# Kernel optimization log

Measured on AMD Instinct MI355X. Metric: run time of the kernel, lower is better.

## Reference

```python
import jax, jax.numpy as jnp
import numpy as np

N_HOPS = 2
TOPK = 10
LAMBDA = 0.5  # lambda_coeff
N_ENT = 8192
N_USR = 16384
CHANNEL = 64
N_EDGE = 1000000
NNZ = 500000
N_REL = 9


def _l2norm(x, eps=1e-12):
    # F.normalize: x / max(||x||, eps) per row
    n = jnp.linalg.norm(x, axis=-1, keepdims=True)
    return x / jnp.maximum(n, eps)


def build_adj(context, topk):
    n = context.shape[0]
    cn = context / jnp.linalg.norm(context, axis=-1, keepdims=True)
    sim = cn @ cn.T                                   # [N,N]
    knn_val, knn_ind = jax.lax.top_k(sim, topk)        # [N,topk]
    rows = jnp.repeat(jnp.arange(n), topk)
    cols = knn_ind.reshape(-1)
    vals = knn_val.reshape(-1)
    rowsum = knn_val.sum(axis=1)                       # sparse row sums
    dinv = rowsum ** -0.5
    vals = dinv[rows] * vals * dinv[cols]              # D^-1/2 A D^-1/2
    return jnp.zeros((n, n), context.dtype).at[rows, cols].add(vals)


def aggregate(entity_emb, user_emb, head, tail, i_rows, i_cols, inter_vals, weight, edge_type):
    n_ent = entity_emb.shape[0]
    n_usr = user_emb.shape[0]
    rel = weight[edge_type - 1]                        # [E,C]
    h_emb = entity_emb[head]
    t_emb = entity_emb[tail]
    neigh = t_emb * rel                                # [E,C]
    # attention weight: (||h*r|| * ||t*r||)^2 per edge
    att = (jnp.linalg.norm(h_emb * rel, axis=1) * jnp.linalg.norm(t_emb * rel, axis=1)) ** 2
    # scatter_softmax over head segments
    m = jax.ops.segment_max(att, head, num_segments=n_ent)
    e = jnp.exp(att - m[head])
    denom = jax.ops.segment_sum(e, head, num_segments=n_ent)
    w = (e / denom[head])[:, None]                     # [E,1], broadcast == expand
    entity_agg = jax.ops.segment_sum(w * neigh, head, num_segments=n_ent)
    # sparse mm: interact_mat @ entity_emb
    user_agg = jax.ops.segment_sum(inter_vals[:, None] * entity_emb[i_cols], i_rows, num_segments=n_usr)
    score = jax.nn.softmax(user_emb @ weight.T, axis=-1)
    user_agg = user_agg + (score @ weight) * user_agg
    return entity_agg, user_agg


def setup_inputs() -> dict:
    key = jax.random.key(0)
    k = jax.random.split(key, 7)
    user_emb = jax.random.normal(k[0], (N_USR, CHANNEL), jnp.float32) * 0.1
    entity_emb = jax.random.normal(k[1], (N_ENT, CHANNEL), jnp.float32) * 0.1
    edge_index = jax.random.randint(k[2], (2, N_EDGE), 0, N_ENT)
    edge_type = jax.random.randint(k[3], (N_EDGE,), 0, N_REL - 1) + 1  # in [1, n_relations-1]
    inter_rows = jax.random.randint(k[4], (NNZ,), 0, N_USR)
    inter_cols = jax.random.randint(k[5], (NNZ,), 0, N_ENT)
    inter_indices = jnp.stack([inter_rows, inter_cols], axis=0)
    inter_vals = jax.random.uniform(k[6], (NNZ,), jnp.float32)
    # xavier-uniform-like relation weight
    bound = float(np.sqrt(6.0 / (N_REL - 1 + CHANNEL)))
    weight = jax.random.uniform(jax.random.fold_in(key, 7), (N_REL - 1, CHANNEL), jnp.float32, -bound, bound)
    return {"user_emb": user_emb, "entity_emb": entity_emb, "edge_index": edge_index,
            "edge_type": edge_type, "inter_indices": inter_indices,
            "inter_vals": inter_vals, "weight": weight}


def reference(user_emb, entity_emb, edge_index, edge_type, inter_indices, inter_vals, weight):
    head, tail = edge_index[0], edge_index[1]
    i_rows, i_cols = inter_indices[0], inter_indices[1]
    origin_item_adj = build_adj(entity_emb, TOPK)
    entity_res_emb = entity_emb
    user_res_emb = user_emb
    for _ in range(N_HOPS):
        entity_emb, user_emb = aggregate(entity_emb, user_emb, head, tail,
                                         i_rows, i_cols, inter_vals, weight, edge_type)
        entity_emb = _l2norm(entity_emb)
        user_emb = _l2norm(user_emb)
        entity_res_emb = entity_res_emb + entity_emb
        user_res_emb = user_res_emb + user_emb
    item_adj = (1.0 - LAMBDA) * build_adj(entity_res_emb, TOPK) + LAMBDA * origin_item_adj
    return entity_res_emb, user_res_emb, item_adj
```

## Files before the change

kernel.cpp:

```cpp
#include <hip/hip_runtime.h>
#include <hip/hip_bf16.h>

#define N_ENT   8192
#define N_USR   16384
#define CH      64
#define N_EDGEC 1000000
#define NNZC    500000
#define TOPKC   10
#define NRELM1  8
#define KSPLIT  384
#define BKS     96
#define LDSP    104
#define NTILE   64

typedef __bf16 bf16x8 __attribute__((ext_vector_type(8)));
typedef float  f32x4  __attribute__((ext_vector_type(4)));

static __device__ __forceinline__ float waveReduceSum(float v){
#pragma unroll
  for(int o=1;o<64;o<<=1) v += __shfl_xor(v,o,64);
  return v;
}
static __device__ __forceinline__ float waveReduceMax(float v){
#pragma unroll
  for(int o=1;o<64;o<<=1) v = fmaxf(v, __shfl_xor(v,o,64));
  return v;
}
static __device__ __forceinline__ unsigned long long u64max(unsigned long long a, unsigned long long b){
  return a>b? a: b;
}
static __device__ __forceinline__ unsigned mapf(float v){
  unsigned u = __float_as_uint(v);
  return (u & 0x80000000u) ? ~u : (u | 0x80000000u);
}
static __device__ __forceinline__ float unmapf(unsigned mk){
  unsigned uo = (mk & 0x80000000u) ? (mk ^ 0x80000000u) : ~mk;
  return __uint_as_float(uo);
}
static __device__ __forceinline__ ushort f2bf(float x){
  unsigned u = __float_as_uint(x);
  return (ushort)((u + 0x7FFFu + ((u>>16)&1u)) >> 16);
}
static __device__ __forceinline__ float bf2f(ushort h){
  return __uint_as_float((unsigned)h<<16);
}

__global__ void k_hist(const int* __restrict__ keys, int n, int* __restrict__ hist){
  int i = blockIdx.x*blockDim.x + threadIdx.x;
  int stride = gridDim.x*blockDim.x;
  for(; i<n; i+=stride) atomicAdd(&hist[keys[i]], 1);
}

__global__ __launch_bounds__(1024) void k_scan(const int* __restrict__ hist,
                                               int* __restrict__ start,
                                               int* __restrict__ cursor, int n){
  __shared__ int part[1024];
  int t = threadIdx.x;
  int chunk = n/1024;
  int base = t*chunk;
  int s = 0;
  for(int i=0;i<chunk;i++) s += hist[base+i];
  part[t] = s; __syncthreads();
  for(int off=1; off<1024; off<<=1){
    int v = (t>=off) ? part[t-off] : 0;
    __syncthreads();
    part[t] += v;
    __syncthreads();
  }
  int run = (t==0) ? 0 : part[t-1];
  for(int i=0;i<chunk;i++){
    start[base+i] = run; cursor[base+i] = run;
    run += hist[base+i];
  }
  if(t==1023) start[n] = run;
}

__global__ void k_scatter_sortE(const int* __restrict__ head,
                                const int* __restrict__ tail,
                                const int* __restrict__ etype, int n,
                                int* __restrict__ cursor, int* __restrict__ trS){
  int i = blockIdx.x*blockDim.x + threadIdx.x;
  int stride = gridDim.x*blockDim.x;
  for(; i<n; i+=stride){
    int pos = atomicAdd(&cursor[head[i]], 1);
    trS[pos] = (tail[i] & 8191) | ((etype[i]-1)<<13);
  }
}

__global__ void k_scatter_sortU(const int* __restrict__ irows,
                                const int* __restrict__ icols,
                                const float* __restrict__ ivals, int n,
                                int* __restrict__ cursor,
                                int* __restrict__ icolsS, float* __restrict__ ivalsS){
  int i = blockIdx.x*blockDim.x + threadIdx.x;
  int stride = gridDim.x*blockDim.x;
  for(; i<n; i+=stride){
    int pos = atomicAdd(&cursor[irows[i]], 1);
    icolsS[pos] = icols[i];
    ivalsS[pos] = ivals[i];
  }
}

__global__ __launch_bounds__(256) void k_split(const float* __restrict__ in,
                                               ushort* __restrict__ outA,
                                               ushort* __restrict__ outB){
  int wave = threadIdx.x>>6, lane = threadIdx.x&63;
  int r = blockIdx.x*4 + wave;
  float v = in[(size_t)r*CH+lane];
  float ss = waveReduceSum(v*v);
  float x = v / sqrtf(ss);
  ushort h = f2bf(x);
  float r1 = x - bf2f(h);
  ushort m = f2bf(r1);
  float r2 = r1 - bf2f(m);
  ushort l = f2bf(r2);
  ushort* oA = outA + (size_t)r*KSPLIT;
  ushort* oB = outB + (size_t)r*KSPLIT;
  oA[lane]     =h; oA[64+lane] =h; oA[128+lane]=m;
  oA[192+lane] =l; oA[256+lane]=h; oA[320+lane]=m;
  oB[lane]     =h; oB[64+lane] =m; oB[128+lane]=h;
  oB[192+lane] =h; oB[256+lane]=l; oB[320+lane]=m;
}

__global__ __launch_bounds__(256) void k_gemm_bf16(const ushort* __restrict__ A,
                                                   const ushort* __restrict__ B,
                                                   float* __restrict__ C,
                                                   float* __restrict__ rowmax){
  __shared__ ushort As[128*LDSP];
  __shared__ ushort Bs[128*LDSP];
  const int tid = threadIdx.x, lane = tid&63, wid = tid>>6;
  const int bi = blockIdx.y*128, bj = blockIdx.x*128;
  const int wr = (wid>>1)*64, wc = (wid&1)*64;
  const int r16 = lane&15, kg = lane>>4;

  f32x4 acc[4][4] = {};

  const uint4* gA = (const uint4*)A + (size_t)bi*(KSPLIT/8);
  const uint4* gB = (const uint4*)B + (size_t)bj*(KSPLIT/8);
  const int row2 = tid>>1, half = tid&1;

  for(int s=0; s<KSPLIT/BKS; ++s){
    __syncthreads();
#pragma unroll
    for(int jj=0;jj<6;jj++){
      *(uint4*)&As[row2*LDSP + half*48 + jj*8] = gA[row2*(KSPLIT/8) + s*12 + half*6 + jj];
      *(uint4*)&Bs[row2*LDSP + half*48 + jj*8] = gB[row2*(KSPLIT/8) + s*12 + half*6 + jj];
    }
    __syncthreads();
#pragma unroll
    for(int kk=0;kk<3;kk++){
      bf16x8 a[4], b[4];
#pragma unroll
      for(int m=0;m<4;m++)
        a[m] = *(const bf16x8*)&As[(wr+m*16+r16)*LDSP + kk*32 + kg*8];
#pragma unroll
      for(int n=0;n<4;n++)
        b[n] = *(const bf16x8*)&Bs[(wc+n*16+r16)*LDSP + kk*32 + kg*8];
#pragma unroll
      for(int m=0;m<4;m++)
#pragma unroll
        for(int n=0;n<4;n++)
          acc[m][n] = __builtin_amdgcn_mfma_f32_16x16x32_bf16(a[m], b[n], acc[m][n], 0,0,0);
    }
  }

#pragma unroll
  for(int m=0;m<4;m++){
#pragma unroll
    for(int n=0;n<4;n++){
      size_t base = (size_t)(bi + wr + m*16 + kg*4)*N_ENT + (bj + wc + n*16 + r16);
      C[base]          = acc[m][n][0];
      C[base+N_ENT]    = acc[m][n][1];
      C[base+2*N_ENT]  = acc[m][n][2];
      C[base+3*N_ENT]  = acc[m][n][3];
    }
  }

  float tmax[4][4];
#pragma unroll
  for(int m=0;m<4;m++){
#pragma unroll
    for(int rg=0;rg<4;rg++){
      float v = acc[m][0][rg];
      v = fmaxf(v, acc[m][1][rg]);
      v = fmaxf(v, acc[m][2][rg]);
      v = fmaxf(v, acc[m][3][rg]);
#pragma unroll
      for(int o=1;o<16;o<<=1) v = fmaxf(v, __shfl_xor(v, o, 64));
      tmax[m][rg] = v;
    }
  }
  __syncthreads();
  float* rm = (float*)As;
  if(((wid&1)==0) && r16==0){
#pragma unroll
    for(int m=0;m<4;m++)
#pragma unroll
      for(int rg=0;rg<4;rg++)
        rm[wr + m*16 + kg*4 + rg] = tmax[m][rg];
  }
  __syncthreads();
  if(((wid&1)==1) && r16==0){
#pragma unroll
    for(int m=0;m<4;m++)
#pragma unroll
      for(int rg=0;rg<4;rg++){
        int rrow = wr + m*16 + kg*4 + rg;
        rowmax[(size_t)(bi+rrow)*NTILE + blockIdx.x] = fmaxf(tmax[m][rg], rm[rrow]);
      }
  }
}

#define CANDCAP 256
__global__ __launch_bounds__(64) void k_topk(const float* __restrict__ S,
                                             const float* __restrict__ rowmax,
                                             int* __restrict__ knn_idx,
                                             float* __restrict__ knn_val,
                                             float* __restrict__ rowsum){
  const int row = blockIdx.x;
  const int lane = threadIdx.x;
  const float4* s4 = (const float4*)(S + (size_t)row*N_ENT);

  __shared__ unsigned long long cand[CANDCAP];
  __shared__ int tlist[NTILE];
  __shared__ int cnt, tcnt;
  if(lane==0){ cnt=0; tcnt=0; }
  __syncthreads();

  float tm = rowmax[(size_t)row*NTILE + lane];
  unsigned long long work = ((unsigned long long)mapf(tm)<<32) | (unsigned)lane;
  unsigned long long w = 0;
  for(int sel=0; sel<TOPKC; ++sel){
    w = work;
#pragma unroll
    for(int o=1;o<64;o<<=1) w = u64max(w, __shfl_xor(w,o,64));
    if(work == w) work = 0ull;
  }
  float tauf = unmapf((unsigned)(w>>32));

  if(tm >= tauf){ int p = atomicAdd(&tcnt,1); tlist[p] = lane; }
  __syncthreads();
  int nt = tcnt;

  for(int i = (lane>>5); i < nt; i += 2){
    int t  = tlist[i];
    int fo = lane&31;
    float4 v = s4[t*32 + fo];
    int c0 = t*128 + fo*4;
    float vv[4] = {v.x,v.y,v.z,v.w};
#pragma unroll
    for(int j=0;j<4;j++){
      if(vv[j] >= tauf){
        int pos = atomicAdd(&cnt,1);
        if(pos < CANDCAP)
          cand[pos] = ((unsigned long long)mapf(vv[j])<<32)
                    | (unsigned long long)(0xFFFFFFFFu - (unsigned)(c0+j));
      }
    }
  }
  __syncthreads();
  int n = cnt;

  if(n <= CANDCAP){
    unsigned long long c0 = (lane      < n) ? cand[lane]       : 0ull;
    unsigned long long c1 = (lane+64   < n) ? cand[lane+64]    : 0ull;
    unsigned long long c2 = (lane+128  < n) ? cand[lane+128]   : 0ull;
    unsigned long long c3 = (lane+192  < n) ? cand[lane+192]   : 0ull;
    float rs = 0.f;
    for(int sel=0; sel<TOPKC; ++sel){
      unsigned long long m = u64max(u64max(c0,c1), u64max(c2,c3));
#pragma unroll
      for(int o=1;o<64;o<<=1) m = u64max(m, __shfl_xor(m,o,64));
      if(c0==m) c0=0ull; else if(c1==m) c1=0ull;
      else if(c2==m) c2=0ull; else if(c3==m) c3=0ull;
      if(lane==0){
        float v = unmapf((unsigned)(m>>32));
        int col = (int)(0xFFFFFFFFu - (unsigned)(m & 0xFFFFFFFFu));
        knn_idx[row*TOPKC+sel] = col;
        knn_val[row*TOPKC+sel] = v;
        rs += v;
      }
    }
    if(lane==0) rowsum[row] = rs;
  } else {
    unsigned long long loc[TOPKC];
#pragma unroll
    for(int i=0;i<TOPKC;i++) loc[i]=0ull;
    for(int it=0; it<N_ENT/256; ++it){
      int vi = it*64+lane;
      float4 v = s4[vi];
      int c0i = vi*4;
      float vv[4] = {v.x,v.y,v.z,v.w};
#pragma unroll
      for(int j=0;j<4;j++){
        unsigned u = mapf(vv[j]);
        unsigned long long key = ((unsigned long long)u<<32)
                               | (unsigned long long)(0xFFFFFFFFu - (unsigned)(c0i+j));
        if(key > loc[TOPKC-1]){
          unsigned long long t = key;
#pragma unroll
          for(int z=0; z<TOPKC; ++z){
            if(t > loc[z]){ unsigned long long tmp=loc[z]; loc[z]=t; t=tmp; }
          }
        }
      }
    }
    float rs = 0.f;
    for(int sel=0; sel<TOPKC; ++sel){
      unsigned long long m = loc[0];
#pragma unroll
      for(int o=1;o<64;o<<=1) m = u64max(m, __shfl_xor(m,o,64));
      if(loc[0] == m){
#pragma unroll
        for(int z=0;z<TOPKC-1;++z) loc[z]=loc[z+1];
        loc[TOPKC-1]=0ull;
      }
      if(lane==0){
        float v = unmapf((unsigned)(m>>32));
        int col = (int)(0xFFFFFFFFu - (unsigned)(m & 0xFFFFFFFFu));
        knn_idx[row*TOPKC+sel] = col;
        knn_val[row*TOPKC+sel] = v;
        rs += v;
      }
    }
    if(lane==0) rowsum[row] = rs;
  }
}

__global__ __launch_bounds__(256) void k_q(const float* __restrict__ ent,
                                           const float* __restrict__ W,
                                           float* __restrict__ q){
  int wave=threadIdx.x>>6, lane=threadIdx.x&63;
  int r = blockIdx.x*4+wave;
  if(r>=N_ENT) return;
  float x = ent[(size_t)r*CH+lane];
#pragma unroll
  for(int rel=0; rel<NRELM1; rel++){
    float tt = x*W[rel*CH+lane];
    float s = waveReduceSum(tt*tt);
    if(lane==0) q[r*NRELM1+rel]=s;
  }
}

__global__ __launch_bounds__(256) void k_edge_agg(
    const int* __restrict__ trS, const int* __restrict__ startE,
    const float* __restrict__ ent, const float* __restrict__ W,
    const float* __restrict__ q, float* __restrict__ wbuf,
    float* __restrict__ agg){
  int wave=threadIdx.x>>6, lane=threadIdx.x&63;
  int h = blockIdx.x*4+wave;
  if(h>=N_ENT) return;
  int s = startE[h], e2 = startE[h+1];

  float qh[NRELM1];
#pragma unroll
  for(int r=0;r<NRELM1;r++) qh[r] = q[h*NRELM1+r];

  float mx = 0.f;
  for(int p=s+lane; p<e2; p+=64){
    int tr = trS[p];
    int tl = tr & 8191, r = tr>>13;
    float att = qh[r]*q[tl*NRELM1+r];
    wbuf[p] = att;
    mx = fmaxf(mx, att);
  }
  mx = waveReduceMax(mx);

  float dn = 0.f;
  for(int p=s+lane; p<e2; p+=64){
    float e = expf(wbuf[p]-mx);
    wbuf[p] = e;
    dn += e;
  }
  dn = waveReduceSum(dn);
  float inv = (dn>0.f) ? 1.f/dn : 0.f;

  float wr[NRELM1];
#pragma unroll
  for(int r=0;r<NRELM1;r++) wr[r] = W[r*CH+lane];
  float acc = 0.f;
  for(int p=s; p<e2; p++){
    int tr = trS[p];
    int tl = tr & 8191, r = tr>>13;
    float wgt = wbuf[p]*inv;
    acc = fmaf(wgt*wr[r], ent[(size_t)tl*CH+lane], acc);
  }
  agg[(size_t)h*CH+lane] = acc;
}

__global__ __launch_bounds__(256) void k_user(
    const int* __restrict__ icolsS, const float* __restrict__ ivalsS,
    const int* __restrict__ startU,
    const float* __restrict__ ent, const float* __restrict__ W,
    float* __restrict__ usr, float* __restrict__ usr_res){
  int wave=threadIdx.x>>6, lane=threadIdx.x&63;
  int u = blockIdx.x*4+wave;
  if(u>=N_USR) return;
  float ue = usr[(size_t)u*CH+lane];
  float l[NRELM1];
#pragma unroll
  for(int r=0;r<NRELM1;r++) l[r] = waveReduceSum(ue*W[r*CH+lane]);
  float lm = l[0];
#pragma unroll
  for(int r=1;r<NRELM1;r++) lm = fmaxf(lm,l[r]);
  float se=0.f;
#pragma unroll
  for(int r=0;r<NRELM1;r++){ l[r]=expf(l[r]-lm); se+=l[r]; }
  float inv = 1.f/se;
  float g = 0.f;
#pragma unroll
  for(int r=0;r<NRELM1;r++) g = fmaf(l[r]*inv, W[r*CH+lane], g);
  float acc=0.f;
  int s=startU[u], e2=startU[u+1];
  for(int p=s;p<e2;p++){
    acc = fmaf(ivalsS[p], ent[(size_t)icolsS[p]*CH+lane], acc);
  }
  float res = acc*(1.f+g);
  float nrm = sqrtf(waveReduceSum(res*res));
  float outv = res / fmaxf(nrm, 1e-12f);
  usr_res[(size_t)u*CH+lane] += outv;
  usr[(size_t)u*CH+lane] = outv;
}

__global__ __launch_bounds__(256) void k_entfin(const float* __restrict__ agg,
                                                float* __restrict__ cur,
                                                float* __restrict__ res){
  int wave=threadIdx.x>>6, lane=threadIdx.x&63;
  int r = blockIdx.x*4+wave;
  if(r>=N_ENT) return;
  float v = agg[(size_t)r*CH+lane];
  float nrm = sqrtf(waveReduceSum(v*v));
  float outv = v / fmaxf(nrm, 1e-12f);
  cur[(size_t)r*CH+lane]=outv;
  res[(size_t)r*CH+lane]+=outv;
}

__global__ __launch_bounds__(256) void k_write_adj(
    const int* __restrict__ ki0, const float* __restrict__ kv0,
    const float* __restrict__ rs0,
    const int* __restrict__ ki1, const float* __restrict__ kv1,
    const float* __restrict__ rs1,
    float* __restrict__ adj){
  const int row = blockIdx.x;
  const int t = threadIdx.x;
  __shared__ int   cols[2*TOPKC];
  __shared__ float vals[2*TOPKC];

  if(t < TOPKC){
    int c = ki1[row*TOPKC+t];
    cols[t] = c;
    vals[t] = 0.5f * kv1[row*TOPKC+t] / (sqrtf(rs1[row]) * sqrtf(rs1[c]));
  } else if(t < 2*TOPKC){
    int i = t - TOPKC;
    int c = ki0[row*TOPKC+i];
    cols[t] = c;
    vals[t] = 0.5f * kv0[row*TOPKC+i] / (sqrtf(rs0[row]) * sqrtf(rs0[c]));
  }
  __syncthreads();
  if(t==0){
    for(int i=TOPKC;i<2*TOPKC;i++){
      int c = cols[i];
      for(int j=0;j<TOPKC;j++){
        if(cols[j]==c){ vals[j]+=vals[i]; cols[i]=-1; break; }
      }
    }
  }
  __syncthreads();

  float4* adj4 = (float4*)(adj + (size_t)row*N_ENT);
  float4 z = {0.f,0.f,0.f,0.f};
#pragma unroll
  for(int k=0;k<8;k++) adj4[k*256 + t] = z;
  __syncthreads();
  if(t < 2*TOPKC){
    int c = cols[t];
    if(c >= 0) adj[(size_t)row*N_ENT + c] = vals[t];
  }
}

extern "C" void kernel_launch(void* const* d_in, const int* in_sizes, int n_in,
                              void* d_out, int out_size, void* d_ws, size_t ws_size,
                              hipStream_t stream){
  const float* user_emb   = (const float*)d_in[0];
  const float* entity_emb = (const float*)d_in[1];
  const int*   edge_index = (const int*)d_in[2];
  const int*   edge_type  = (const int*)d_in[3];
  const int*   inter_idx  = (const int*)d_in[4];
  const float* inter_vals = (const float*)d_in[5];
  const float* W          = (const float*)d_in[6];

  const int* head  = edge_index;
  const int* tail  = edge_index + N_EDGEC;
  const int* irows = inter_idx;
  const int* icols = inter_idx + NNZC;

  float* out     = (float*)d_out;
  float* ent_res = out;
  float* usr_res = out + (size_t)N_ENT*CH;
  float* adj     = out + (size_t)N_ENT*CH + (size_t)N_USR*CH;

  char* wp = (char*)d_ws;
  auto alloc = [&](size_t bytes)->void*{
    void* p = (void*)wp; wp += (bytes+255)/256*256; return p;
  };
  ushort* abufA  = (ushort*)alloc((size_t)N_ENT*KSPLIT*2);
  ushort* abufB  = (ushort*)alloc((size_t)N_ENT*KSPLIT*2);
  float* rowmax  = (float*)alloc((size_t)N_ENT*NTILE*4);
  float* cur_ent = (float*)alloc((size_t)N_ENT*CH*4);
  float* cur_usr = (float*)alloc((size_t)N_USR*CH*4);
  float* agg     = (float*)alloc((size_t)N_ENT*CH*4);
  float* q       = (float*)alloc((size_t)N_ENT*NRELM1*4);
  int*   histE   = (int*)alloc((size_t)N_ENT*4);
  int*   startE  = (int*)alloc((size_t)(N_ENT+1)*4);
  int*   cursorE = (int*)alloc((size_t)N_ENT*4);
  int*   trS     = (int*)alloc((size_t)N_EDGEC*4);
  int*   histU   = (int*)alloc((size_t)N_USR*4);
  int*   startU  = (int*)alloc((size_t)(N_USR+1)*4);
  int*   cursorU = (int*)alloc((size_t)N_USR*4);
  int*   icolsS  = (int*)alloc((size_t)NNZC*4);
  float* ivalsS  = (float*)alloc((size_t)NNZC*4);
  int*   knn_idx0= (int*)alloc((size_t)N_ENT*TOPKC*4);
  float* knn_val0= (float*)alloc((size_t)N_ENT*TOPKC*4);
  float* rowsum0 = (float*)alloc((size_t)N_ENT*4);
  int*   knn_idx1= (int*)alloc((size_t)N_ENT*TOPKC*4);
  float* knn_val1= (float*)alloc((size_t)N_ENT*TOPKC*4);
  float* rowsum1 = (float*)alloc((size_t)N_ENT*4);

  float* wbuf = adj;

  hipMemsetAsync(histE, 0, (size_t)N_ENT*4, stream);
  hipMemsetAsync(histU, 0, (size_t)N_USR*4, stream);
  hipMemcpyAsync(ent_res, entity_emb, (size_t)N_ENT*CH*4, hipMemcpyDeviceToDevice, stream);
  hipMemcpyAsync(usr_res, user_emb,   (size_t)N_USR*CH*4, hipMemcpyDeviceToDevice, stream);
  hipMemcpyAsync(cur_ent, entity_emb, (size_t)N_ENT*CH*4, hipMemcpyDeviceToDevice, stream);
  hipMemcpyAsync(cur_usr, user_emb,   (size_t)N_USR*CH*4, hipMemcpyDeviceToDevice, stream);

  k_hist<<<1024,256,0,stream>>>(head, N_EDGEC, histE);
  k_hist<<<512,256,0,stream>>>(irows, NNZC, histU);
  k_scan<<<1,1024,0,stream>>>(histE, startE, cursorE, N_ENT);
  k_scan<<<1,1024,0,stream>>>(histU, startU, cursorU, N_USR);
  k_scatter_sortE<<<1024,256,0,stream>>>(head, tail, edge_type, N_EDGEC, cursorE, trS);
  k_scatter_sortU<<<512,256,0,stream>>>(irows, icols, inter_vals, NNZC, cursorU, icolsS, ivalsS);

  dim3 gg(N_ENT/128, N_ENT/128);

  k_split<<<N_ENT/4,256,0,stream>>>(entity_emb, abufA, abufB);
  k_gemm_bf16<<<gg,256,0,stream>>>(abufA, abufB, adj, rowmax);
  k_topk<<<N_ENT,64,0,stream>>>(adj, rowmax, knn_idx0, knn_val0, rowsum0);

  for(int hop=0; hop<2; ++hop){
    k_q<<<N_ENT/4,256,0,stream>>>(cur_ent, W, q);
    k_edge_agg<<<N_ENT/4,256,0,stream>>>(trS, startE, cur_ent, W, q, wbuf, agg);
    k_user<<<N_USR/4,256,0,stream>>>(icolsS, ivalsS, startU, cur_ent, W, cur_usr, usr_res);
    k_entfin<<<N_ENT/4,256,0,stream>>>(agg, cur_ent, ent_res);
  }

  k_split<<<N_ENT/4,256,0,stream>>>(ent_res, abufA, abufB);
  k_gemm_bf16<<<gg,256,0,stream>>>(abufA, abufB, adj, rowmax);
  k_topk<<<N_ENT,64,0,stream>>>(adj, rowmax, knn_idx1, knn_val1, rowsum1);

  k_write_adj<<<N_ENT,256,0,stream>>>(knn_idx0, knn_val0, rowsum0,
                                      knn_idx1, knn_val1, rowsum1, adj);
}
```

Measured before the change: 839.3 us.

## Exploit similarity symmetry by computing only upper-triangle GEMM tiles

```diff
diff --git a/kernel.cpp b/kernel.cpp
--- a/kernel.cpp
+++ b/kernel.cpp
@@ -11,7 +11,9 @@
 #define KSPLIT  384
 #define BKS     96
 #define LDSP    104
+#define LDSTP   133
 #define NTILE   64
+#define NTRI    2080
 
 typedef __bf16 bf16x8 __attribute__((ext_vector_type(8)));
 typedef float  f32x4  __attribute__((ext_vector_type(4)));
@@ -126,10 +128,17 @@
                                                    const ushort* __restrict__ B,
                                                    float* __restrict__ C,
                                                    float* __restrict__ rowmax){
-  __shared__ ushort As[128*LDSP];
-  __shared__ ushort Bs[128*LDSP];
+  __shared__ __align__(16) ushort As[128*LDSP];
+  __shared__ __align__(16) ushort Bs[128*LDSP];
   const int tid = threadIdx.x, lane = tid&63, wid = tid>>6;
-  const int bi = blockIdx.y*128, bj = blockIdx.x*128;
+
+  int bid = blockIdx.x;
+  int by = (int)((129.0f - sqrtf(16641.0f - 8.0f*(float)bid)) * 0.5f);
+  while(((by+1)*64 - ((by+1)*by)/2) <= bid) by++;
+  while((by*64 - (by*(by-1))/2) > bid) by--;
+  int bx = by + (bid - (by*64 - (by*(by-1))/2));
+
+  const int bi = by*128, bj = bx*128;
   const int wr = (wid>>1)*64, wc = (wid&1)*64;
   const int r16 = lane&15, kg = lane>>4;
 
@@ -190,8 +199,22 @@
       tmax[m][rg] = v;
     }
   }
-  __syncthreads();
-  float* rm = (float*)As;
+  float cm[4];
+#pragma unroll
+  for(int n=0;n<4;n++){
+    float v = acc[0][n][0];
+#pragma unroll
+    for(int m=0;m<4;m++)
+#pragma unroll
+      for(int rg=0;rg<4;rg++) v = fmaxf(v, acc[m][n][rg]);
+    v = fmaxf(v, __shfl_xor(v, 16, 64));
+    v = fmaxf(v, __shfl_xor(v, 32, 64));
+    cm[n] = v;
+  }
+
+  __syncthreads();
+  float* rm  = (float*)Bs;
+  float* cmb = ((float*)Bs) + 128;
   if(((wid&1)==0) && r16==0){
 #pragma unroll
     for(int m=0;m<4;m++)
@@ -199,6 +222,10 @@
       for(int rg=0;rg<4;rg++)
         rm[wr + m*16 + kg*4 + rg] = tmax[m][rg];
   }
+  if(wid<2 && kg==0){
+#pragma unroll
+    for(int n=0;n<4;n++) cmb[wc + n*16 + r16] = cm[n];
+  }
   __syncthreads();
   if(((wid&1)==1) && r16==0){
 #pragma unroll
@@ -206,8 +233,43 @@
 #pragma unroll
       for(int rg=0;rg<4;rg++){
         int rrow = wr + m*16 + kg*4 + rg;
-        rowmax[(size_t)(bi+rrow)*NTILE + blockIdx.x] = fmaxf(tmax[m][rg], rm[rrow]);
-      }
+        rowmax[(size_t)(bi+rrow)*NTILE + bx] = fmaxf(tmax[m][rg], rm[rrow]);
+      }
+  }
+  if(by != bx && wid>=2 && kg==0){
+#pragma unroll
+    for(int n=0;n<4;n++){
+      int ccol = wc + n*16 + r16;
+      rowmax[(size_t)(bj+ccol)*NTILE + by] = fmaxf(cm[n], cmb[ccol]);
+    }
+  }
+
+  if(by != bx){
+    float* ldsT = (float*)As;
+    for(int q=0;q<4;q++){
+      __syncthreads();
+#pragma unroll
+      for(int n=0;n<4;n++){
+        if(((wc>>5) + (n>>1)) == q){
+          int cl = ((n&1)*16) + r16;
+#pragma unroll
+          for(int m=0;m<4;m++)
+#pragma unroll
+            for(int rg=0;rg<4;rg++)
+              ldsT[cl*LDSTP + wr + m*16 + kg*4 + rg] = acc[m][n][rg];
+        }
+      }
+      __syncthreads();
+      int cr = tid>>3;
+      int g  = tid&7;
+      float* crow = C + (size_t)(bj + q*32 + cr)*N_ENT + bi;
+#pragma unroll
+      for(int f=0; f<4; ++f){
+        int cidx = (g + f*8)*4;
+        float4 v = *(float4*)&ldsT[cr*LDSTP + cidx];
+        *(float4*)&crow[cidx] = v;
+      }
+    }
   }
 }
 
@@ -542,10 +604,8 @@
   k_scatter_sortE<<<1024,256,0,stream>>>(head, tail, edge_type, N_EDGEC, cursorE, trS);
   k_scatter_sortU<<<512,256,0,stream>>>(irows, icols, inter_vals, NNZC, cursorU, icolsS, ivalsS);
 
-  dim3 gg(N_ENT/128, N_ENT/128);
-
   k_split<<<N_ENT/4,256,0,stream>>>(entity_emb, abufA, abufB);
-  k_gemm_bf16<<<gg,256,0,stream>>>(abufA, abufB, adj, rowmax);
+  k_gemm_bf16<<<NTRI,256,0,stream>>>(abufA, abufB, adj, rowmax);
   k_topk<<<N_ENT,64,0,stream>>>(adj, rowmax, knn_idx0, knn_val0, rowsum0);
 
   for(int hop=0; hop<2; ++hop){
@@ -556,7 +616,7 @@
   }
 
   k_split<<<N_ENT/4,256,0,stream>>>(ent_res, abufA, abufB);
-  k_gemm_bf16<<<gg,256,0,stream>>>(abufA, abufB, adj, rowmax);
+  k_gemm_bf16<<<NTRI,256,0,stream>>>(abufA, abufB, adj, rowmax);
   k_topk<<<N_ENT,64,0,stream>>>(adj, rowmax, knn_idx1, knn_val1, rowsum1);
 
   k_write_adj<<<N_ENT,256,0,stream>>>(knn_idx0, knn_val0, rowsum0,
```

Result: no change. 826.5 us (-1.5%).
